# Optimization experiments

Hardware: AMD Instinct MI355X
Metric: run time of the kernel (lower is better)

The kernel has to match this reference:

```python
import jax, jax.numpy as jnp
import numpy as np

N, F, H, E = 131072, 128, 128, 2097152
FC, FC1, A = 256, 256, 128
NEG_SLOPE = 0.01

def _lrelu(v):
    return jnp.where(v >= 0, v, NEG_SLOPE * v)

def setup_inputs() -> dict:
    key = jax.random.key(0)
    ks = jax.random.split(key, 12)
    s = lambda fan: 1.0 / np.sqrt(fan)
    return {
        "x": jax.random.normal(ks[0], (N, F), dtype=jnp.float32),
        "edge_index": jax.random.randint(ks[1], (2, E), 0, N, dtype=jnp.int64),
        "W": jax.random.normal(ks[2], (F, H), jnp.float32) * s(F),
        "b": jnp.zeros((H,), jnp.float32),
        "w1a": jax.random.normal(ks[3], (H, FC1), jnp.float32) * s(H),
        "b1a": jnp.zeros((FC1,), jnp.float32),
        "w1b": jax.random.normal(ks[4], (FC1, A), jnp.float32) * s(FC1),
        "b1b": jnp.zeros((A,), jnp.float32),
        "w2a": jax.random.normal(ks[5], (H, FC), jnp.float32) * s(H),
        "b2a": jnp.zeros((FC,), jnp.float32),
        "w2b": jax.random.normal(ks[6], (FC, A), jnp.float32) * s(FC),
        "b2b": jnp.zeros((A,), jnp.float32),
    }

def reference(x, edge_index, W, b, w1a, b1a, w1b, b1b, w2a, b2a, w2b, b2b):
    n = x.shape[0]
    # GCNConv: linear transform first
    h = x @ W  # [N, H]
    # add self loops
    loop = jnp.arange(n, dtype=edge_index.dtype)
    src = jnp.concatenate([edge_index[0], loop])
    dst = jnp.concatenate([edge_index[1], loop])
    # symmetric normalization with unit edge weights
    deg = jax.ops.segment_sum(jnp.ones_like(src, dtype=h.dtype), dst, num_segments=n)
    dinv = jnp.where(deg > 0, deg ** -0.5, 0.0)
    norm = dinv[src] * dinv[dst]  # [E+N]
    msg = h[src] * norm[:, None]  # [E+N, H] gather
    out = jax.ops.segment_sum(msg, dst, num_segments=n) + b  # scatter-add
    out = _lrelu(out)
    out = out.reshape(-1, F, H).mean(axis=1)  # [B, H] mean-pool over the F nodes per graph
    x1 = _lrelu(out @ w1a + b1a) @ w1b + b1b
    x2 = _lrelu(out @ w2a + b2a) @ w2b + b2b
    return (x1, x2)
```

## Files before the change

kernel.cpp:

```cpp
#include <hip/hip_runtime.h>

#define NEG_SLOPE 0.01f
#define BCAP 3072
#define CSTRIDE 16
#define BLKB 1024
#define EPTB 16

typedef __attribute__((ext_vector_type(8))) short bh8;
typedef __attribute__((ext_vector_type(4))) float f4acc;
typedef __attribute__((ext_vector_type(2))) float f2v;

static __device__ __forceinline__ float lrelu(float v) {
    return v >= 0.0f ? v : NEG_SLOPE * v;
}

static __device__ __forceinline__ unsigned short bf16of(float a) {
    unsigned u = __float_as_uint(a);
    return (unsigned short)((u + 0x7FFFu + ((u >> 16) & 1u)) >> 16);
}
static __device__ __forceinline__ unsigned pack_bf16(float a, float b) {
    return (unsigned)bf16of(a) | ((unsigned)bf16of(b) << 16);
}

__global__ __launch_bounds__(BLKB) void k_bucket(const int* __restrict__ edge, int E, int B,
                                                 int* __restrict__ bcnt, int* __restrict__ buckets) {
    __shared__ int hist[1024];
    __shared__ int rbase[1024];
    int tid = threadIdx.x;
    if (tid < B) hist[tid] = 0;
    __syncthreads();

    int start = blockIdx.x * (BLKB * EPTB) + tid * EPTB;
    int entry[EPTB];
    int gg[EPTB];
    int nloc = 0;

    if (start + EPTB <= E) {
#pragma unroll
        for (int q = 0; q < EPTB / 4; ++q) {
            int4 s4 = *(const int4*)&edge[start + q * 4];
            int4 d4 = *(const int4*)&edge[E + start + q * 4];
            entry[q * 4 + 0] = (s4.x << 7) | (d4.x & 127); gg[q * 4 + 0] = d4.x >> 7;
            entry[q * 4 + 1] = (s4.y << 7) | (d4.y & 127); gg[q * 4 + 1] = d4.y >> 7;
            entry[q * 4 + 2] = (s4.z << 7) | (d4.z & 127); gg[q * 4 + 2] = d4.z >> 7;
            entry[q * 4 + 3] = (s4.w << 7) | (d4.w & 127); gg[q * 4 + 3] = d4.w >> 7;
        }
        nloc = EPTB;
    } else {
#pragma unroll
        for (int i = 0; i < EPTB; ++i) {
            if (start + i < E) {
                int s = edge[start + i], d = edge[E + start + i];
                entry[i] = (s << 7) | (d & 127);
                gg[i] = d >> 7;
                nloc = i + 1;
            }
        }
    }
#pragma unroll
    for (int i = 0; i < EPTB; ++i)
        if (i < nloc) atomicAdd(&hist[gg[i]], 1);
    __syncthreads();

    if (tid < B) {
        int c = hist[tid];
        rbase[tid] = (c > 0) ? atomicAdd(&bcnt[tid * CSTRIDE], c) : 0;
        hist[tid] = 0;
    }
    __syncthreads();

#pragma unroll
    for (int i = 0; i < EPTB; ++i) {
        if (i < nloc) {
            int g = gg[i];
            int pos = rbase[g] + atomicAdd(&hist[g], 1);
            if (pos < BCAP) buckets[(size_t)g * BCAP + pos] = entry[i];
        }
    }
}

__global__ __launch_bounds__(256) void k_deg(const int* __restrict__ buckets,
                                             const int* __restrict__ bcnt,
                                             float* __restrict__ dinv) {
    __shared__ int c[128];
    int g = blockIdx.x, tid = threadIdx.x;
    if (tid < 128) c[tid] = 0;
    __syncthreads();
    int m = min(bcnt[g * CSTRIDE], BCAP);
    const int* bk = &buckets[(size_t)g * BCAP];
    int m4 = m >> 2;
    for (int i = tid; i < m4; i += 256) {
        int4 e = ((const int4*)bk)[i];
        atomicAdd(&c[e.x & 127], 1);
        atomicAdd(&c[e.y & 127], 1);
        atomicAdd(&c[e.z & 127], 1);
        atomicAdd(&c[e.w & 127], 1);
    }
    for (int i = (m4 << 2) + tid; i < m; i += 256) atomicAdd(&c[bk[i] & 127], 1);
    __syncthreads();
    if (tid < 128) dinv[g * 128 + tid] = rsqrtf((float)(c[tid] + 1));
}

__global__ __launch_bounds__(128) void k_wt(const float* __restrict__ W,
                                            unsigned short* __restrict__ Wt) {
    int c = blockIdx.x;
    int k = threadIdx.x;
    Wt[c * 128 + k] = bf16of(W[k * 128 + c]);
}

#define GBM 64
__global__ __launch_bounds__(256) void k_gemm(const float* __restrict__ x,
                                              const unsigned short* __restrict__ Wt,
                                              const float* __restrict__ dinv,
                                              unsigned* __restrict__ h8) {
    int tid = threadIdx.x;
    int wave = tid >> 6;
    int lane = tid & 63;
    long r0 = (long)blockIdx.x * GBM;
    int arow = (int)r0 + wave * 16 + (lane & 15);
    int kbase = (lane >> 4) * 8;
    int l15 = lane & 15;

    union { uint4 u; bh8 h; } cv;

    bh8 af[4];
#pragma unroll
    for (int kb = 0; kb < 4; ++kb) {
        const float* px = &x[(size_t)arow * 128 + kb * 32 + kbase];
        float4 a0 = *(const float4*)px;
        float4 a1 = *(const float4*)(px + 4);
        cv.u.x = pack_bf16(a0.x, a0.y);
        cv.u.y = pack_bf16(a0.z, a0.w);
        cv.u.z = pack_bf16(a1.x, a1.y);
        cv.u.w = pack_bf16(a1.z, a1.w);
        af[kb] = cv.h;
    }

    f4acc acc[8];
#pragma unroll
    for (int ct = 0; ct < 8; ++ct) acc[ct] = (f4acc){0.f, 0.f, 0.f, 0.f};

#pragma unroll
    for (int kb = 0; kb < 4; ++kb) {
#pragma unroll
        for (int ct = 0; ct < 8; ++ct) {
            int col = ct * 16 + l15;
            bh8 bf = *(const bh8*)&Wt[col * 128 + kb * 32 + kbase];
            acc[ct] = __builtin_amdgcn_mfma_f32_16x16x32_bf16(af[kb], bf, acc[ct], 0, 0, 0);
        }
    }

    int rbase = wave * 16 + (lane >> 4) * 4;
    float dr[4];
#pragma unroll
    for (int r = 0; r < 4; ++r) dr[r] = dinv[r0 + rbase + r];
#pragma unroll
    for (int r = 0; r < 4; ++r) {
        long row = r0 + rbase + r;
        unsigned w0 = __builtin_amdgcn_cvt_pk_fp8_f32(acc[0][r] * dr[r], acc[1][r] * dr[r], 0, false);
        w0 = __builtin_amdgcn_cvt_pk_fp8_f32(acc[2][r] * dr[r], acc[3][r] * dr[r], w0, true);
        unsigned w1 = __builtin_amdgcn_cvt_pk_fp8_f32(acc[4][r] * dr[r], acc[5][r] * dr[r], 0, false);
        w1 = __builtin_amdgcn_cvt_pk_fp8_f32(acc[6][r] * dr[r], acc[7][r] * dr[r], w1, true);
        uint2 pw; pw.x = w0; pw.y = w1;
        ((uint2*)&h8[row * 32])[l15] = pw;
    }
}

__global__ __launch_bounds__(512) void k_aggr(const unsigned* __restrict__ h8,
                                              const int* __restrict__ buckets,
                                              const int* __restrict__ bcnt,
                                              const float* __restrict__ bias,
                                              float* __restrict__ pooled) {
    __shared__ int cnt[128];
    __shared__ int incl[128];
    __shared__ int head[128];
    __shared__ int sorted[BCAP];
    __shared__ float red[8][128];
    int tid = threadIdx.x;
    int wave = tid >> 6;
    int lane = tid & 63;
    int g = blockIdx.x;
    int m = min(bcnt[g * CSTRIDE], BCAP);
    const int* gbk = &buckets[(size_t)g * BCAP];

    if (tid < 128) cnt[tid] = 0;
    __syncthreads();
    for (int i = tid; i < m; i += 512) atomicAdd(&cnt[gbk[i] & 127], 1);
    __syncthreads();
    if (tid < 128) incl[tid] = cnt[tid];
    __syncthreads();
    for (int off = 1; off < 128; off <<= 1) {
        int t = (tid < 128 && tid >= off) ? incl[tid - off] : 0;
        __syncthreads();
        if (tid < 128) incl[tid] += t;
        __syncthreads();
    }
    if (tid < 128) head[tid] = incl[tid] - cnt[tid];
    __syncthreads();
    for (int i = tid; i < m; i += 512) {
        int e = gbk[i];
        int p = atomicAdd(&head[e & 127], 1);
        sorted[p] = e;
    }
    __syncthreads();

    int m2 = lane & 31;
    int half = lane >> 5;
    int fb = (m2 >> 1) + 64 * (m2 & 1);
    f2v b0, b1;
    b0.x = bias[fb];      b0.y = bias[fb + 16];
    b1.x = bias[fb + 32]; b1.y = bias[fb + 48];
    f2v acc0 = {0.f, 0.f}, acc1 = {0.f, 0.f};

#pragma unroll 1
    for (int t = 0; t < 16; ++t) {
        int d = wave * 16 + t;
        int re = incl[d];
        int rs = re - cnt[d];
        int v = g * 128 + d;
        unsigned selfw = h8[(size_t)v * 32 + m2];
        f2v p0 = {0.f, 0.f}, p1 = {0.f, 0.f};

        int nfull = (re - rs) & ~7;
        int i = rs;
        for (; i < rs + nfull; i += 8) {
            int e0 = sorted[i + half];
            int e1 = sorted[i + 2 + half];
            int e2 = sorted[i + 4 + half];
            int e3 = sorted[i + 6 + half];
            unsigned u0 = h8[(size_t)(e0 >> 7) * 32 + m2];
            unsigned u1 = h8[(size_t)(e1 >> 7) * 32 + m2];
            unsigned u2 = h8[(size_t)(e2 >> 7) * 32 + m2];
            unsigned u3 = h8[(size_t)(e3 >> 7) * 32 + m2];
            p0 += __builtin_amdgcn_cvt_pk_f32_fp8(u0, false);
            p1 += __builtin_amdgcn_cvt_pk_f32_fp8(u0, true);
            p0 += __builtin_amdgcn_cvt_pk_f32_fp8(u1, false);
            p1 += __builtin_amdgcn_cvt_pk_f32_fp8(u1, true);
            p0 += __builtin_amdgcn_cvt_pk_f32_fp8(u2, false);
            p1 += __builtin_amdgcn_cvt_pk_f32_fp8(u2, true);
            p0 += __builtin_amdgcn_cvt_pk_f32_fp8(u3, false);
            p1 += __builtin_amdgcn_cvt_pk_f32_fp8(u3, true);
        }
        for (; i < re; i += 2) {
            int i0 = i + half;
            int ic = min(i0, re - 1);
            float w = (i0 < re) ? 1.0f : 0.0f;
            int e = sorted[ic];
            unsigned u = h8[(size_t)(e >> 7) * 32 + m2];
            f2v a = __builtin_amdgcn_cvt_pk_f32_fp8(u, false);
            f2v bqq = __builtin_amdgcn_cvt_pk_f32_fp8(u, true);
            p0 += a * w;
            p1 += bqq * w;
        }

        p0.x += __shfl_xor(p0.x, 32); p0.y += __shfl_xor(p0.y, 32);
        p1.x += __shfl_xor(p1.x, 32); p1.y += __shfl_xor(p1.y, 32);
        f2v s0 = __builtin_amdgcn_cvt_pk_f32_fp8(selfw, false);
        f2v s1 = __builtin_amdgcn_cvt_pk_f32_fp8(selfw, true);
        float dv = rsqrtf((float)(cnt[d] + 1));
        f2v r0v = (p0 + s0) * dv + b0;
        f2v r1v = (p1 + s1) * dv + b1;
        acc0.x += lrelu(r0v.x); acc0.y += lrelu(r0v.y);
        acc1.x += lrelu(r1v.x); acc1.y += lrelu(r1v.y);
    }

    if (lane < 32) {
        red[wave][fb]      = acc0.x;
        red[wave][fb + 16] = acc0.y;
        red[wave][fb + 32] = acc1.x;
        red[wave][fb + 48] = acc1.y;
    }
    __syncthreads();
    if (wave == 0) {
        float tx = 0.0f, ty = 0.0f;
#pragma unroll
        for (int w = 0; w < 8; ++w) {
            tx += red[w][lane];
            ty += red[w][lane + 64];
        }
        pooled[(size_t)g * 128 + lane]      = tx * (1.0f / 128.0f);
        pooled[(size_t)g * 128 + lane + 64] = ty * (1.0f / 128.0f);
    }
}

#define RB 4
__global__ __launch_bounds__(256) void k_mlp(const float* __restrict__ pooled,
                                             const float* __restrict__ w1a, const float* __restrict__ b1a,
                                             const float* __restrict__ w1b, const float* __restrict__ b1b,
                                             const float* __restrict__ w2a, const float* __restrict__ b2a,
                                             const float* __restrict__ w2b, const float* __restrict__ b2b,
                                             float* __restrict__ out, int B) {
    __shared__ float row[RB][128];
    __shared__ float hid[2][RB][256];
    int tid = threadIdx.x;
    int g0 = blockIdx.x * RB;

    for (int i = tid; i < RB * 128; i += 256)
        row[i >> 7][i & 127] = pooled[(size_t)g0 * 128 + i];
    __syncthreads();

    float a1[RB], a2[RB];
#pragma unroll
    for (int r = 0; r < RB; ++r) { a1[r] = 0.0f; a2[r] = 0.0f; }
    for (int k = 0; k < 128; ++k) {
        float wv1 = w1a[k * 256 + tid];
        float wv2 = w2a[k * 256 + tid];
#pragma unroll
        for (int r = 0; r < RB; ++r) {
            float xv = row[r][k];
            a1[r] += xv * wv1;
            a2[r] += xv * wv2;
        }
    }
    float bb1 = b1a[tid], bb2 = b2a[tid];
#pragma unroll
    for (int r = 0; r < RB; ++r) {
        hid[0][r][tid] = lrelu(a1[r] + bb1);
        hid[1][r][tid] = lrelu(a2[r] + bb2);
    }
    __syncthreads();

    int p = tid >> 7;
    int i = tid & 127;
    const float* wb = p ? w2b : w1b;
    const float* bvp = p ? b2b : b1b;
    float o[RB];
#pragma unroll
    for (int r = 0; r < RB; ++r) o[r] = 0.0f;
    for (int k = 0; k < 256; ++k) {
        float wv = wb[k * 128 + i];
#pragma unroll
        for (int r = 0; r < RB; ++r) o[r] += hid[p][r][k] * wv;
    }
    float bias = bvp[i];
#pragma unroll
    for (int r = 0; r < RB; ++r)
        out[(size_t)p * B * 128 + (size_t)(g0 + r) * 128 + i] = o[r] + bias;
}

extern "C" void kernel_launch(void* const* d_in, const int* in_sizes, int n_in,
                              void* d_out, int out_size, void* d_ws, size_t ws_size,
                              hipStream_t stream) {
    const float* x    = (const float*)d_in[0];
    const int*   edge = (const int*)d_in[1];
    const float* W    = (const float*)d_in[2];
    const float* b    = (const float*)d_in[3];
    const float* w1a  = (const float*)d_in[4];
    const float* b1a  = (const float*)d_in[5];
    const float* w1b  = (const float*)d_in[6];
    const float* b1b  = (const float*)d_in[7];
    const float* w2a  = (const float*)d_in[8];
    const float* b2a  = (const float*)d_in[9];
    const float* w2b  = (const float*)d_in[10];
    const float* b2b  = (const float*)d_in[11];

    int n = in_sizes[0] / 128;
    int E = in_sizes[1] / 2;
    int B = n / 128;

    char* ws = (char*)d_ws;
    size_t off = 0;
    auto alloc = [&](size_t bytes) -> void* {
        void* p = ws + off;
        off = (off + bytes + 255) & ~(size_t)255;
        return p;
    };
    unsigned*       h8      = (unsigned*)alloc((size_t)n * 32 * 4);
    int*            buckets = (int*)alloc((size_t)B * BCAP * 4);
    int*            bcnt    = (int*)alloc((size_t)B * CSTRIDE * 4);
    float*          dinv    = (float*)alloc((size_t)n * 4);
    float*          pooled  = (float*)alloc((size_t)B * 128 * 4);
    unsigned short* Wt      = (unsigned short*)alloc(128 * 128 * 2);
    (void)ws_size; (void)n_in; (void)out_size;

    int bblk = (E + BLKB * EPTB - 1) / (BLKB * EPTB);

    hipMemsetAsync(bcnt, 0, (size_t)B * CSTRIDE * 4, stream);
    hipLaunchKernelGGL(k_wt,     dim3(128), dim3(128), 0, stream, W, Wt);
    hipLaunchKernelGGL(k_bucket, dim3(bblk), dim3(BLKB), 0, stream, edge, E, B, bcnt, buckets);
    hipLaunchKernelGGL(k_deg,    dim3(B), dim3(256), 0, stream, buckets, bcnt, dinv);
    hipLaunchKernelGGL(k_gemm,   dim3(n / GBM), dim3(256), 0, stream, x, Wt, dinv, h8);
    hipLaunchKernelGGL(k_aggr,   dim3(B), dim3(512), 0, stream, h8, buckets, bcnt, b, pooled);
    hipLaunchKernelGGL(k_mlp,    dim3(B / RB), dim3(256), 0, stream,
                       pooled, w1a, b1a, w1b, b1b, w2a, b2a, w2b, b2b, (float*)d_out, B);
}
```

Baseline: 142.7 us.

## Interleave two destination nodes in aggregation and cache bucket entries in registers

The aggregation kernel now handles two destination nodes per iteration with interleaved gather loops, which raises memory-level parallelism. Bucket entries are kept in registers between the counting pass and the sorting pass, and byte offsets are precomputed so the global bucket is read once and the address math is simpler. The bcnt memset is folded into the weight-transpose kernel to save an API call, and the MLP rows per block go from 4 to 8. The costs are higher register pressure and a hard limit of 6*512 entries per bucket. The fused zeroing only covers bcnt when B*CSTRIDE equals 128*128.

```diff
diff --git a/kernel.cpp b/kernel.cpp
--- a/kernel.cpp
+++ b/kernel.cpp
@@ -102,10 +102,12 @@
 }
 
 __global__ __launch_bounds__(128) void k_wt(const float* __restrict__ W,
-                                            unsigned short* __restrict__ Wt) {
+                                            unsigned short* __restrict__ Wt,
+                                            int* __restrict__ bcnt) {
     int c = blockIdx.x;
     int k = threadIdx.x;
     Wt[c * 128 + k] = bf16of(W[k * 128 + c]);
+    bcnt[c * 128 + k] = 0;
 }
 
 #define GBM 64
@@ -185,7 +187,14 @@
 
     if (tid < 128) cnt[tid] = 0;
     __syncthreads();
-    for (int i = tid; i < m; i += 512) atomicAdd(&cnt[gbk[i] & 127], 1);
+    int myent[6];
+#pragma unroll
+    for (int j = 0; j < 6; ++j) {
+        int i = tid + j * 512;
+        int e = (i < m) ? gbk[i] : -1;
+        myent[j] = e;
+        if (e >= 0) atomicAdd(&cnt[e & 127], 1);
+    }
     __syncthreads();
     if (tid < 128) incl[tid] = cnt[tid];
     __syncthreads();
@@ -197,15 +206,19 @@
     }
     if (tid < 128) head[tid] = incl[tid] - cnt[tid];
     __syncthreads();
-    for (int i = tid; i < m; i += 512) {
-        int e = gbk[i];
-        int p = atomicAdd(&head[e & 127], 1);
-        sorted[p] = e;
+#pragma unroll
+    for (int j = 0; j < 6; ++j) {
+        int e = myent[j];
+        if (e >= 0) {
+            int p = atomicAdd(&head[e & 127], 1);
+            sorted[p] = e & ~127;
+        }
     }
     __syncthreads();
 
     int m2 = lane & 31;
     int half = lane >> 5;
+    const char* pb = (const char*)h8 + (m2 << 2);
     int fb = (m2 >> 1) + 64 * (m2 & 1);
     f2v b0, b1;
     b0.x = bias[fb];      b0.y = bias[fb + 16];
@@ -213,55 +226,127 @@
     f2v acc0 = {0.f, 0.f}, acc1 = {0.f, 0.f};
 
 #pragma unroll 1
-    for (int t = 0; t < 16; ++t) {
-        int d = wave * 16 + t;
-        int re = incl[d];
-        int rs = re - cnt[d];
-        int v = g * 128 + d;
-        unsigned selfw = h8[(size_t)v * 32 + m2];
-        f2v p0 = {0.f, 0.f}, p1 = {0.f, 0.f};
-
-        int nfull = (re - rs) & ~7;
-        int i = rs;
-        for (; i < rs + nfull; i += 8) {
-            int e0 = sorted[i + half];
-            int e1 = sorted[i + 2 + half];
-            int e2 = sorted[i + 4 + half];
-            int e3 = sorted[i + 6 + half];
-            unsigned u0 = h8[(size_t)(e0 >> 7) * 32 + m2];
-            unsigned u1 = h8[(size_t)(e1 >> 7) * 32 + m2];
-            unsigned u2 = h8[(size_t)(e2 >> 7) * 32 + m2];
-            unsigned u3 = h8[(size_t)(e3 >> 7) * 32 + m2];
-            p0 += __builtin_amdgcn_cvt_pk_f32_fp8(u0, false);
-            p1 += __builtin_amdgcn_cvt_pk_f32_fp8(u0, true);
-            p0 += __builtin_amdgcn_cvt_pk_f32_fp8(u1, false);
-            p1 += __builtin_amdgcn_cvt_pk_f32_fp8(u1, true);
-            p0 += __builtin_amdgcn_cvt_pk_f32_fp8(u2, false);
-            p1 += __builtin_amdgcn_cvt_pk_f32_fp8(u2, true);
-            p0 += __builtin_amdgcn_cvt_pk_f32_fp8(u3, false);
-            p1 += __builtin_amdgcn_cvt_pk_f32_fp8(u3, true);
-        }
-        for (; i < re; i += 2) {
-            int i0 = i + half;
-            int ic = min(i0, re - 1);
-            float w = (i0 < re) ? 1.0f : 0.0f;
-            int e = sorted[ic];
-            unsigned u = h8[(size_t)(e >> 7) * 32 + m2];
-            f2v a = __builtin_amdgcn_cvt_pk_f32_fp8(u, false);
-            f2v bqq = __builtin_amdgcn_cvt_pk_f32_fp8(u, true);
-            p0 += a * w;
-            p1 += bqq * w;
-        }
-
-        p0.x += __shfl_xor(p0.x, 32); p0.y += __shfl_xor(p0.y, 32);
-        p1.x += __shfl_xor(p1.x, 32); p1.y += __shfl_xor(p1.y, 32);
-        f2v s0 = __builtin_amdgcn_cvt_pk_f32_fp8(selfw, false);
-        f2v s1 = __builtin_amdgcn_cvt_pk_f32_fp8(selfw, true);
-        float dv = rsqrtf((float)(cnt[d] + 1));
-        f2v r0v = (p0 + s0) * dv + b0;
-        f2v r1v = (p1 + s1) * dv + b1;
-        acc0.x += lrelu(r0v.x); acc0.y += lrelu(r0v.y);
-        acc1.x += lrelu(r1v.x); acc1.y += lrelu(r1v.y);
+    for (int t = 0; t < 8; ++t) {
+        int dA = wave * 16 + t * 2;
+        int dB = dA + 1;
+        int reA = incl[dA], csA = cnt[dA], rsA = reA - csA;
+        int reB = incl[dB], csB = cnt[dB], rsB = reB - csB;
+        unsigned selfA = *(const unsigned*)(pb + ((size_t)(g * 128 + dA) << 7));
+        unsigned selfB = *(const unsigned*)(pb + ((size_t)(g * 128 + dB) << 7));
+        f2v pA0 = {0.f, 0.f}, pA1 = {0.f, 0.f};
+        f2v pB0 = {0.f, 0.f}, pB1 = {0.f, 0.f};
+        int iA = rsA, iB = rsB;
+        int endA8 = rsA + ((reA - rsA) & ~7);
+        int endB8 = rsB + ((reB - rsB) & ~7);
+
+        while (iA < endA8 && iB < endB8) {
+            int a0 = sorted[iA + half];
+            int a1 = sorted[iA + 2 + half];
+            int a2 = sorted[iA + 4 + half];
+            int a3 = sorted[iA + 6 + half];
+            int o0 = sorted[iB + half];
+            int o1 = sorted[iB + 2 + half];
+            int o2 = sorted[iB + 4 + half];
+            int o3 = sorted[iB + 6 + half];
+            unsigned uA0 = *(const unsigned*)(pb + a0);
+            unsigned uA1 = *(const unsigned*)(pb + a1);
+            unsigned uA2 = *(const unsigned*)(pb + a2);
+            unsigned uA3 = *(const unsigned*)(pb + a3);
+            unsigned uB0 = *(const unsigned*)(pb + o0);
+            unsigned uB1 = *(const unsigned*)(pb + o1);
+            unsigned uB2 = *(const unsigned*)(pb + o2);
+            unsigned uB3 = *(const unsigned*)(pb + o3);
+            pA0 += __builtin_amdgcn_cvt_pk_f32_fp8(uA0, false);
+            pA1 += __builtin_amdgcn_cvt_pk_f32_fp8(uA0, true);
+            pA0 += __builtin_amdgcn_cvt_pk_f32_fp8(uA1, false);
+            pA1 += __builtin_amdgcn_cvt_pk_f32_fp8(uA1, true);
+            pA0 += __builtin_amdgcn_cvt_pk_f32_fp8(uA2, false);
+            pA1 += __builtin_amdgcn_cvt_pk_f32_fp8(uA2, true);
+            pA0 += __builtin_amdgcn_cvt_pk_f32_fp8(uA3, false);
+            pA1 += __builtin_amdgcn_cvt_pk_f32_fp8(uA3, true);
+            pB0 += __builtin_amdgcn_cvt_pk_f32_fp8(uB0, false);
+            pB1 += __builtin_amdgcn_cvt_pk_f32_fp8(uB0, true);
+            pB0 += __builtin_amdgcn_cvt_pk_f32_fp8(uB1, false);
+            pB1 += __builtin_amdgcn_cvt_pk_f32_fp8(uB1, true);
+            pB0 += __builtin_amdgcn_cvt_pk_f32_fp8(uB2, false);
+            pB1 += __builtin_amdgcn_cvt_pk_f32_fp8(uB2, true);
+            pB0 += __builtin_amdgcn_cvt_pk_f32_fp8(uB3, false);
+            pB1 += __builtin_amdgcn_cvt_pk_f32_fp8(uB3, true);
+            iA += 8; iB += 8;
+        }
+        while (iA < endA8) {
+            int a0 = sorted[iA + half];
+            int a1 = sorted[iA + 2 + half];
+            int a2 = sorted[iA + 4 + half];
+            int a3 = sorted[iA + 6 + half];
+            unsigned uA0 = *(const unsigned*)(pb + a0);
+            unsigned uA1 = *(const unsigned*)(pb + a1);
+            unsigned uA2 = *(const unsigned*)(pb + a2);
+            unsigned uA3 = *(const unsigned*)(pb + a3);
+            pA0 += __builtin_amdgcn_cvt_pk_f32_fp8(uA0, false);
+            pA1 += __builtin_amdgcn_cvt_pk_f32_fp8(uA0, true);
+            pA0 += __builtin_amdgcn_cvt_pk_f32_fp8(uA1, false);
+            pA1 += __builtin_amdgcn_cvt_pk_f32_fp8(uA1, true);
+            pA0 += __builtin_amdgcn_cvt_pk_f32_fp8(uA2, false);
+            pA1 += __builtin_amdgcn_cvt_pk_f32_fp8(uA2, true);
+            pA0 += __builtin_amdgcn_cvt_pk_f32_fp8(uA3, false);
+            pA1 += __builtin_amdgcn_cvt_pk_f32_fp8(uA3, true);
+            iA += 8;
+        }
+        while (iB < endB8) {
+            int o0 = sorted[iB + half];
+            int o1 = sorted[iB + 2 + half];
+            int o2 = sorted[iB + 4 + half];
+            int o3 = sorted[iB + 6 + half];
+            unsigned uB0 = *(const unsigned*)(pb + o0);
+            unsigned uB1 = *(const unsigned*)(pb + o1);
+            unsigned uB2 = *(const unsigned*)(pb + o2);
+            unsigned uB3 = *(const unsigned*)(pb + o3);
+            pB0 += __builtin_amdgcn_cvt_pk_f32_fp8(uB0, false);
+            pB1 += __builtin_amdgcn_cvt_pk_f32_fp8(uB0, true);
+            pB0 += __builtin_amdgcn_cvt_pk_f32_fp8(uB1, false);
+            pB1 += __builtin_amdgcn_cvt_pk_f32_fp8(uB1, true);
+            pB0 += __builtin_amdgcn_cvt_pk_f32_fp8(uB2, false);
+            pB1 += __builtin_amdgcn_cvt_pk_f32_fp8(uB2, true);
+            pB0 += __builtin_amdgcn_cvt_pk_f32_fp8(uB3, false);
+            pB1 += __builtin_amdgcn_cvt_pk_f32_fp8(uB3, true);
+            iB += 8;
+        }
+        for (; iA < reA; iA += 2) {
+            int i0 = iA + half;
+            int ic = min(i0, reA - 1);
+            float w = (i0 < reA) ? 1.0f : 0.0f;
+            unsigned u = *(const unsigned*)(pb + sorted[ic]);
+            pA0 += __builtin_amdgcn_cvt_pk_f32_fp8(u, false) * w;
+            pA1 += __builtin_amdgcn_cvt_pk_f32_fp8(u, true) * w;
+        }
+        for (; iB < reB; iB += 2) {
+            int i0 = iB + half;
+            int ic = min(i0, reB - 1);
+            float w = (i0 < reB) ? 1.0f : 0.0f;
+            unsigned u = *(const unsigned*)(pb + sorted[ic]);
+            pB0 += __builtin_amdgcn_cvt_pk_f32_fp8(u, false) * w;
+            pB1 += __builtin_amdgcn_cvt_pk_f32_fp8(u, true) * w;
+        }
+
+        pA0.x += __shfl_xor(pA0.x, 32); pA0.y += __shfl_xor(pA0.y, 32);
+        pA1.x += __shfl_xor(pA1.x, 32); pA1.y += __shfl_xor(pA1.y, 32);
+        pB0.x += __shfl_xor(pB0.x, 32); pB0.y += __shfl_xor(pB0.y, 32);
+        pB1.x += __shfl_xor(pB1.x, 32); pB1.y += __shfl_xor(pB1.y, 32);
+        f2v sA0 = __builtin_amdgcn_cvt_pk_f32_fp8(selfA, false);
+        f2v sA1 = __builtin_amdgcn_cvt_pk_f32_fp8(selfA, true);
+        f2v sB0 = __builtin_amdgcn_cvt_pk_f32_fp8(selfB, false);
+        f2v sB1 = __builtin_amdgcn_cvt_pk_f32_fp8(selfB, true);
+        float dvA = rsqrtf((float)(csA + 1));
+        float dvB = rsqrtf((float)(csB + 1));
+        f2v rA0 = (pA0 + sA0) * dvA + b0;
+        f2v rA1 = (pA1 + sA1) * dvA + b1;
+        f2v rB0 = (pB0 + sB0) * dvB + b0;
+        f2v rB1 = (pB1 + sB1) * dvB + b1;
+        acc0.x += lrelu(rA0.x) + lrelu(rB0.x);
+        acc0.y += lrelu(rA0.y) + lrelu(rB0.y);
+        acc1.x += lrelu(rA1.x) + lrelu(rB1.x);
+        acc1.y += lrelu(rA1.y) + lrelu(rB1.y);
     }
 
     if (lane < 32) {
@@ -283,7 +368,7 @@
     }
 }
 
-#define RB 4
+#define RB 8
 __global__ __launch_bounds__(256) void k_mlp(const float* __restrict__ pooled,
                                              const float* __restrict__ w1a, const float* __restrict__ b1a,
                                              const float* __restrict__ w1b, const float* __restrict__ b1b,
@@ -375,8 +460,7 @@
 
     int bblk = (E + BLKB * EPTB - 1) / (BLKB * EPTB);
 
-    hipMemsetAsync(bcnt, 0, (size_t)B * CSTRIDE * 4, stream);
-    hipLaunchKernelGGL(k_wt,     dim3(128), dim3(128), 0, stream, W, Wt);
+    hipLaunchKernelGGL(k_wt,     dim3(128), dim3(128), 0, stream, W, Wt, bcnt);
     hipLaunchKernelGGL(k_bucket, dim3(bblk), dim3(BLKB), 0, stream, edge, E, B, bcnt, buckets);
     hipLaunchKernelGGL(k_deg,    dim3(B), dim3(256), 0, stream, buckets, bcnt, dinv);
     hipLaunchKernelGGL(k_gemm,   dim3(n / GBM), dim3(256), 0, stream, x, Wt, dinv, h8);
```

New measurement: 167.1 us. 1.17x slower.
